# Performance work log

Measured on AMD Instinct MI355X. Metric: run time of the kernel, lower is better.

The kernel has to match this reference:

```python
import jax, jax.numpy as jnp
import numpy as np
from jax import lax

BATCH = 8192
PATCH = 2
STRIDE = 2
OUT_CH = 4
NUM_PATCHES = ((28 - PATCH) // STRIDE + 1) ** 2  # 196
THRESHOLD = 0.8
EPS = 1e-12


def setup_inputs() -> dict:
    key = jax.random.key(0)
    k1, k2, k3, k4, k5 = jax.random.split(key, 5)
    x = jax.random.normal(k1, (BATCH, 1, 28, 28), dtype=jnp.float32)
    conv_w = jax.random.normal(k2, (OUT_CH, 1, PATCH, PATCH), dtype=jnp.float32) * 0.5
    conv_b = jax.random.normal(k3, (OUT_CH,), dtype=jnp.float32) * 0.1
    feat_dim = OUT_CH * NUM_PATCHES + NUM_PATCHES  # 784 + 196 = 980
    lin_w = jax.random.normal(k4, (10, feat_dim), dtype=jnp.float32) * 0.02
    lin_b = jax.random.normal(k5, (10,), dtype=jnp.float32) * 0.01
    return {"x": x, "conv_w": conv_w, "conv_b": conv_b, "lin_w": lin_w, "lin_b": lin_b}


def reference(x, conv_w, conv_b, lin_w, lin_b):
    # conv patch embed: (B,1,28,28) -> (B,C,14,14)
    f = lax.conv_general_dilated(
        x, conv_w, window_strides=(STRIDE, STRIDE), padding="VALID",
        dimension_numbers=("NCHW", "OIHW", "NCHW"))
    f = f + conv_b[None, :, None, None]
    B = f.shape[0]
    flat = f.reshape(B, -1)  # (B, C*P) channel-major, matches torch .view
    # replicate feat.view(num_patches, -1): rows of length C from the flat vector
    pf = flat.reshape(B, NUM_PATCHES, -1)  # (B, P, C)
    nrm = pf / (jnp.linalg.norm(pf, axis=-1, keepdims=True) + EPS)
    # squared cosine similarity = state fidelity, all pairs at once
    fid = jnp.einsum("bpc,bqc->bpq", nrm, nrm) ** 2  # (B, P, P)
    w = (fid >= THRESHOLD).astype(flat.dtype)
    w = w * (1.0 - jnp.eye(NUM_PATCHES, dtype=flat.dtype))  # no self-edges
    deg = jnp.sum(w, axis=-1)  # weighted degree per node, (B, P)
    feats = jnp.concatenate([flat, deg], axis=1)  # (B, 980)
    logits = feats @ lin_w.T + lin_b
    return jax.nn.log_softmax(logits, axis=-1)
```

## Files before the change

kernel.cpp:

```cpp
#include <hip/hip_runtime.h>
#include <math.h>


#define NP 196
#define FEAT 980
#define COS_TH 0.894427190999915878f

typedef short v4s  __attribute__((ext_vector_type(4)));
typedef short v8s  __attribute__((ext_vector_type(8)));
typedef float v16f __attribute__((ext_vector_type(16)));

__global__ __launch_bounds__(256, 6) void quanv_kernel(
    const float* __restrict__ x,
    const float* __restrict__ conv_w,
    const float* __restrict__ conv_b,
    const float* __restrict__ lin_w,
    const float* __restrict__ lin_b,
    float* __restrict__ out)
{
    __shared__ __align__(16) float s_x[2][784];
    __shared__ __align__(16) short s_P[2][224][8];
    __shared__ __align__(16) float s_feats[2][FEAT];

    const int b = blockIdx.x;
    const int t = threadIdx.x;
    const int w = t >> 6, l = t & 63;

    if (t < NP) {
        ((float4*)s_x[0])[t] = ((const float4*)(x + (size_t)(2 * b)     * 784))[t];
        ((float4*)s_x[1])[t] = ((const float4*)(x + (size_t)(2 * b + 1) * 784))[t];
    }
    __syncthreads();

    if (t < NP) {
        int h = t / 14, ww = t - 14 * (t / 14);
        #pragma unroll
        for (int img = 0; img < 2; ++img) {
            const float* r0 = s_x[img] + (2 * h) * 28 + 2 * ww;
            float x00 = r0[0], x01 = r0[1], x10 = r0[28], x11 = r0[29];
            #pragma unroll
            for (int c = 0; c < 4; ++c) {
                float f = conv_b[c]
                        + conv_w[c * 4 + 0] * x00 + conv_w[c * 4 + 1] * x01
                        + conv_w[c * 4 + 2] * x10 + conv_w[c * 4 + 3] * x11;
                s_feats[img][c * NP + t] = f;
            }
        }
    }
    __syncthreads();

    if (t < 224) {
        #pragma unroll
        for (int img = 0; img < 2; ++img) {
            v8s pk = {0, 0, 0, 0, 0, 0, 0, 0};
            if (t < NP) {
                float4 v = ((const float4*)s_feats[img])[t];
                float n = sqrtf(v.x * v.x + v.y * v.y + v.z * v.z + v.w * v.w);
                float inv = 1.0f / (n + 1e-12f);
                float e[4] = { v.x * inv, v.y * inv, v.z * inv, v.w * inv };
                #pragma unroll
                for (int k = 0; k < 4; ++k) {
                    uint32_t bx = __float_as_uint(e[k]);
                    uint32_t rh = bx + 0x7FFFu + ((bx >> 16) & 1u);
                    uint32_t hk = rh >> 16;
                    float hif = __uint_as_float(hk << 16);
                    float res = e[k] - hif;
                    uint32_t br = __float_as_uint(res);
                    uint32_t rl = br + 0x7FFFu + ((br >> 16) & 1u);
                    pk[k]     = (short)hk;
                    pk[4 + k] = (short)(rl >> 16);
                }
            }
            *(v8s*)&s_P[img][t][0] = pk;
        }
    }
    __syncthreads();

    v16f zacc = {0.f,0.f,0.f,0.f,0.f,0.f,0.f,0.f,
                 0.f,0.f,0.f,0.f,0.f,0.f,0.f,0.f};
    asm("" : "+v"(zacc));

    const int ln = l & 31, half = l >> 5;
    #pragma unroll
    for (int jj = 0; jj < 4; ++jj) {
        const int job = w + 4 * jj;
        if (job < 14) {
            const int img = (job >= 7) ? 1 : 0;
            const int j = job - 7 * img;
            const short* Pbase = &s_P[img][0][0];

            v4s bh = *(const v4s*)(Pbase + (32 * j + ln) * 8 + 4 * half);
            v8s B = __builtin_shufflevector(bh, bh, 0, 1, 2, 3, 0, 1, 2, 3);

            unsigned c0 = 0u, c1 = 0u;
            #pragma unroll
            for (int i = 0; i < 6; ++i) {
                v8s A = *(const v8s*)(Pbase + (32 * i + ln) * 8);
                v16f acc = __builtin_amdgcn_mfma_f32_32x32x16_bf16(A, B, zacc, 0, 0, 0);
                #pragma unroll
                for (int e = 0; e < 16; e += 2) {
                    c0 += (fabsf(acc[e])     >= COS_TH) ? 1u : 0u;
                    c1 += (fabsf(acc[e + 1]) >= COS_TH) ? 1u : 0u;
                }
            }
            {
                v8s A = *(const v8s*)(Pbase + (32 * 6 + ln) * 8);
                v16f acc = __builtin_amdgcn_mfma_f32_32x32x16_bf16(A, B, zacc, 0, 0, 0);
                if (half == 0) {
                    c0 += (fabsf(acc[0]) >= COS_TH) ? 1u : 0u;
                    c1 += (fabsf(acc[1]) >= COS_TH) ? 1u : 0u;
                    c0 += (fabsf(acc[2]) >= COS_TH) ? 1u : 0u;
                    c1 += (fabsf(acc[3]) >= COS_TH) ? 1u : 0u;
                }
            }
            unsigned cnt = c0 + c1;
            cnt += __shfl_down(cnt, 32, 64);
            if (l < 32) {
                int col = 32 * j + l;
                if (col < NP)
                    s_feats[img][784 + col] = (float)(int)cnt - 1.0f;
            }
        }
    }
    __syncthreads();

    if (t < 250) {
        int k = t / 25, c = t - 25 * (t / 25);
        const float4* wrow = (const float4*)(lin_w + k * FEAT);
        const float4* f0p = (const float4*)s_feats[0];
        const float4* f1p = (const float4*)s_feats[1];
        float a0 = 0.0f, a1 = 0.0f;
        for (int i = c; i < 245; i += 25) {
            float4 wv = wrow[i];
            float4 f0 = f0p[i];
            float4 f1 = f1p[i];
            a0 = fmaf(f0.x, wv.x, a0); a1 = fmaf(f1.x, wv.x, a1);
            a0 = fmaf(f0.y, wv.y, a0); a1 = fmaf(f1.y, wv.y, a1);
            a0 = fmaf(f0.z, wv.z, a0); a1 = fmaf(f1.z, wv.z, a1);
            a0 = fmaf(f0.w, wv.w, a0); a1 = fmaf(f1.w, wv.w, a1);
        }
        (s_x[0] + 256)[t] = a0;
        (s_x[1] + 256)[t] = a1;
    }
    __syncthreads();

    if (t < 20) {
        int img = t / 10, k = t - 10 * (t / 10);
        const float* part = s_x[img] + 256;
        float s = lin_b[k];
        #pragma unroll
        for (int i = 0; i < 25; ++i) s += part[k * 25 + i];
        (s_x[img] + 512)[k] = s;
    }
    __syncthreads();

    if (t < 20) {
        int img = t / 10, k = t - 10 * (t / 10);
        const float* lg = s_x[img] + 512;
        float m = -INFINITY;
        #pragma unroll
        for (int j2 = 0; j2 < 10; ++j2) m = fmaxf(m, lg[j2]);
        float s = 0.0f;
        #pragma unroll
        for (int j2 = 0; j2 < 10; ++j2) s += expf(lg[j2] - m);
        out[(size_t)(2 * b + img) * 10 + k] = lg[k] - m - logf(s);
    }
}

extern "C" void kernel_launch(void* const* d_in, const int* in_sizes, int n_in,
                              void* d_out, int out_size, void* d_ws, size_t ws_size,
                              hipStream_t stream) {
    const float* x      = (const float*)d_in[0];
    const float* conv_w = (const float*)d_in[1];
    const float* conv_b = (const float*)d_in[2];
    const float* lin_w  = (const float*)d_in[3];
    const float* lin_b  = (const float*)d_in[4];
    float* out = (float*)d_out;
    quanv_kernel<<<dim3(4096), dim3(256), 0, stream>>>(x, conv_w, conv_b, lin_w, lin_b, out);
}
```

Measured before the change: 107.3 us.

## Split tail patch rows from MFMA degree jobs into scalar ballot path

The MFMA pass now covers only the first 192 columns per image in 12 jobs (three per wave) instead of 14 padded jobs. The last four patches of each image are computed by plain FMA dot products against all rows, with ballot popcount for their own degree and LDS atomics to credit the symmetric counts back to the other rows. The aim is to cut the padded, mostly wasted seventh MFMA job and the load imbalance across waves. In exchange it adds LDS atomics, an extra sync and a re-summing pass, and the symmetric split-bf16 dot in fp32 may threshold slightly differently than the MFMA result.

Measured after the change: 104.4 us. 1.03x faster.

```diff
diff --git a/kernel.cpp b/kernel.cpp
--- a/kernel.cpp
+++ b/kernel.cpp
@@ -9,6 +9,10 @@
 typedef short v4s  __attribute__((ext_vector_type(4)));
 typedef short v8s  __attribute__((ext_vector_type(8)));
 typedef float v16f __attribute__((ext_vector_type(16)));
+
+static __device__ __forceinline__ float bf2f(short s) {
+    return __uint_as_float(((uint32_t)(uint16_t)s) << 16);
+}
 
 __global__ __launch_bounds__(256, 6) void quanv_kernel(
     const float* __restrict__ x,
@@ -19,8 +23,13 @@
     float* __restrict__ out)
 {
     __shared__ __align__(16) float s_x[2][784];
-    __shared__ __align__(16) short s_P[2][224][8];
+    __shared__ __align__(16) short s_P[2][256][8];
     __shared__ __align__(16) float s_feats[2][FEAT];
+
+    int*   s_deg    = (int*)s_x;
+    int*   s_cred   = s_deg + 384;
+    float* s_part   = (float*)(s_cred + 392);
+    float* s_logits = s_part + 500;
 
     const int b = blockIdx.x;
     const int t = threadIdx.x;
@@ -49,7 +58,7 @@
     }
     __syncthreads();
 
-    if (t < 224) {
+    {
         #pragma unroll
         for (int img = 0; img < 2; ++img) {
             v8s pk = {0, 0, 0, 0, 0, 0, 0, 0};
@@ -73,6 +82,7 @@
             }
             *(v8s*)&s_P[img][t][0] = pk;
         }
+        if (t < NP) { s_cred[t] = 0; s_cred[196 + t] = 0; }
     }
     __syncthreads();
 
@@ -81,46 +91,65 @@
     asm("" : "+v"(zacc));
 
     const int ln = l & 31, half = l >> 5;
+
     #pragma unroll
-    for (int jj = 0; jj < 4; ++jj) {
+    for (int jj = 0; jj < 3; ++jj) {
         const int job = w + 4 * jj;
-        if (job < 14) {
-            const int img = (job >= 7) ? 1 : 0;
-            const int j = job - 7 * img;
-            const short* Pbase = &s_P[img][0][0];
-
-            v4s bh = *(const v4s*)(Pbase + (32 * j + ln) * 8 + 4 * half);
-            v8s B = __builtin_shufflevector(bh, bh, 0, 1, 2, 3, 0, 1, 2, 3);
-
-            unsigned c0 = 0u, c1 = 0u;
+        const int img = (job >= 6) ? 1 : 0;
+        const int j = job - 6 * img;
+        const short* Pbase = &s_P[img][0][0];
+
+        v4s bh = *(const v4s*)(Pbase + (32 * j + ln) * 8 + 4 * half);
+        v8s B = __builtin_shufflevector(bh, bh, 0, 1, 2, 3, 0, 1, 2, 3);
+
+        unsigned c0 = 0u, c1 = 0u;
+        #pragma unroll
+        for (int i = 0; i < 6; ++i) {
+            v8s A = *(const v8s*)(Pbase + (32 * i + ln) * 8);
+            v16f acc = __builtin_amdgcn_mfma_f32_32x32x16_bf16(A, B, zacc, 0, 0, 0);
             #pragma unroll
-            for (int i = 0; i < 6; ++i) {
-                v8s A = *(const v8s*)(Pbase + (32 * i + ln) * 8);
-                v16f acc = __builtin_amdgcn_mfma_f32_32x32x16_bf16(A, B, zacc, 0, 0, 0);
-                #pragma unroll
-                for (int e = 0; e < 16; e += 2) {
-                    c0 += (fabsf(acc[e])     >= COS_TH) ? 1u : 0u;
-                    c1 += (fabsf(acc[e + 1]) >= COS_TH) ? 1u : 0u;
-                }
+            for (int e = 0; e < 16; e += 2) {
+                c0 += (fabsf(acc[e])     >= COS_TH) ? 1u : 0u;
+                c1 += (fabsf(acc[e + 1]) >= COS_TH) ? 1u : 0u;
             }
-            {
-                v8s A = *(const v8s*)(Pbase + (32 * 6 + ln) * 8);
-                v16f acc = __builtin_amdgcn_mfma_f32_32x32x16_bf16(A, B, zacc, 0, 0, 0);
-                if (half == 0) {
-                    c0 += (fabsf(acc[0]) >= COS_TH) ? 1u : 0u;
-                    c1 += (fabsf(acc[1]) >= COS_TH) ? 1u : 0u;
-                    c0 += (fabsf(acc[2]) >= COS_TH) ? 1u : 0u;
-                    c1 += (fabsf(acc[3]) >= COS_TH) ? 1u : 0u;
-                }
-            }
-            unsigned cnt = c0 + c1;
-            cnt += __shfl_down(cnt, 32, 64);
-            if (l < 32) {
-                int col = 32 * j + l;
-                if (col < NP)
-                    s_feats[img][784 + col] = (float)(int)cnt - 1.0f;
-            }
-        }
+        }
+        unsigned cnt = c0 + c1;
+        cnt += __shfl_down(cnt, 32, 64);
+        if (l < 32)
+            s_deg[img * 192 + 32 * j + l] = (int)cnt;
+    }
+
+    #pragma unroll
+    for (int img = 0; img < 2; ++img) {
+        const int r = 192 + w;
+        const short* pr = &s_P[img][r][0];
+        float pe0 = bf2f(pr[0]) + bf2f(pr[4]);
+        float pe1 = bf2f(pr[1]) + bf2f(pr[5]);
+        float pe2 = bf2f(pr[2]) + bf2f(pr[6]);
+        float pe3 = bf2f(pr[3]) + bf2f(pr[7]);
+        unsigned total = 0u;
+        #pragma unroll
+        for (int k = 0; k < 4; ++k) {
+            int q = 64 * k + l;
+            const short* qr = &s_P[img][q][0];
+            float d =          pe0 * (bf2f(qr[0]) + bf2f(qr[4]));
+            d = fmaf(pe1, bf2f(qr[1]) + bf2f(qr[5]), d);
+            d = fmaf(pe2, bf2f(qr[2]) + bf2f(qr[6]), d);
+            d = fmaf(pe3, bf2f(qr[3]) + bf2f(qr[7]), d);
+            bool hit = fabsf(d) >= COS_TH;
+            unsigned long long m = __ballot(hit);
+            total += (unsigned)__popcll(m);
+            if (hit && q < 192)
+                atomicAdd(&s_cred[img * 196 + q], 1);
+        }
+        if (l == 0)
+            s_feats[img][784 + r] = (float)(int)total - 1.0f;
+    }
+    __syncthreads();
+
+    if (t < 192) {
+        s_feats[0][784 + t] = (float)(s_deg[t]       + s_cred[t])       - 1.0f;
+        s_feats[1][784 + t] = (float)(s_deg[192 + t] + s_cred[196 + t]) - 1.0f;
     }
     __syncthreads();
 
@@ -139,24 +168,24 @@
             a0 = fmaf(f0.z, wv.z, a0); a1 = fmaf(f1.z, wv.z, a1);
             a0 = fmaf(f0.w, wv.w, a0); a1 = fmaf(f1.w, wv.w, a1);
         }
-        (s_x[0] + 256)[t] = a0;
-        (s_x[1] + 256)[t] = a1;
+        s_part[t]       = a0;
+        s_part[250 + t] = a1;
     }
     __syncthreads();
 
     if (t < 20) {
         int img = t / 10, k = t - 10 * (t / 10);
-        const float* part = s_x[img] + 256;
+        const float* part = s_part + 250 * img;
         float s = lin_b[k];
         #pragma unroll
         for (int i = 0; i < 25; ++i) s += part[k * 25 + i];
-        (s_x[img] + 512)[k] = s;
+        s_logits[10 * img + k] = s;
     }
     __syncthreads();
 
     if (t < 20) {
         int img = t / 10, k = t - 10 * (t / 10);
-        const float* lg = s_x[img] + 512;
+        const float* lg = s_logits + 10 * img;
         float m = -INFINITY;
         #pragma unroll
         for (int j2 = 0; j2 < 10; ++j2) m = fmaxf(m, lg[j2]);
```
